# Kernel tuning notes

Measured on AMD Instinct MI355X. Metric: run time of the kernel, lower is better.

The kernel has to match this reference:

```python
import jax, jax.numpy as jnp
import numpy as np

B, D, OUT = 8192, 1024, 256
H1, H2 = 8, 4
EPS = 1e-5


def setup_inputs() -> dict:
    key = jax.random.key(0)
    ks = jax.random.split(key, 8)
    sc = lambda k, shape: jax.random.normal(k, shape, jnp.float32) * 0.05
    return {
        "x": jax.random.normal(ks[0], (B, D), jnp.float32),
        "W1": sc(ks[1], (D, H1, 1)),      # D diagonal blocks of the masked Linear(D -> 8D)
        "b1": sc(ks[2], (D * H1,)),
        "g1": jnp.ones((D * H1,), jnp.float32),
        "be1": jnp.zeros((D * H1,), jnp.float32),
        "W2": sc(ks[3], (D, H2, H1)),     # D diagonal blocks of the masked Linear(8D -> 4D)
        "b2": sc(ks[4], (D * H2,)),
        "g2": jnp.ones((D * H2,), jnp.float32),
        "be2": jnp.zeros((D * H2,), jnp.float32),
        "Wfc": sc(ks[5], (OUT, D * H2)),
        "bfc": sc(ks[6], (OUT,)),
    }


def _batchnorm(h, g, b):
    # BatchNorm1d in training mode: per-channel batch mean, biased variance
    mu = h.mean(axis=0)
    var = h.var(axis=0)  # ddof=0 (biased), matching torch normalization
    return g * (h - mu) * jax.lax.rsqrt(var + EPS) + b


def reference(x, W1, b1, g1, be1, W2, b2, g2, be2, Wfc, bfc):
    n = x.shape[0]
    # layer 1: per-feature (1 -> H1) block GEMM == masked dense Linear
    h = jnp.einsum("bdi,doi->bdo", x[:, :, None], W1).reshape(n, D * H1)
    h = jax.nn.relu(_batchnorm(h + b1, g1, be1))
    # layer 2: per-feature (H1 -> H2) block GEMM
    h = jnp.einsum("bdi,doi->bdo", h.reshape(n, D, H1), W2).reshape(n, D * H2)
    h = jax.nn.relu(_batchnorm(h + b2, g2, be2))
    # dense output head
    return h @ Wfc.T + bfc
```

## Files before the change

### kernel.cpp

```cpp
#include <hip/hip_runtime.h>

#define EPSV 1e-5f

typedef short bf16x8 __attribute__((ext_vector_type(8)));
typedef float f32x4 __attribute__((ext_vector_type(4)));

static __device__ __forceinline__ unsigned short f2b(float f) {
  union { float f; unsigned u; } v; v.f = f;
  return (unsigned short)((v.u + 0x7fffu + ((v.u >> 16) & 1u)) >> 16);
}

__global__ void k_pre(const float* __restrict__ wfc, unsigned short* __restrict__ wb,
                      const float* __restrict__ x, float* __restrict__ ps1) {
  if (blockIdx.x < 512) {
    const int f = blockIdx.x * 256 + threadIdx.x;
    const int l15 = f & 15, quad = (f >> 4) & 3, nb = (f >> 6) & 15, k32b = f >> 10;
    const int n = nb * 16 + l15;
    const int k = k32b * 32 + quad * 8;
    const float4* src = (const float4*)(wfc + (size_t)n * 4096 + k);
    float4 a = src[0], b = src[1];
    ushort4 o0, o1;
    o0.x = f2b(a.x); o0.y = f2b(a.y); o0.z = f2b(a.z); o0.w = f2b(a.w);
    o1.x = f2b(b.x); o1.y = f2b(b.y); o1.z = f2b(b.z); o1.w = f2b(b.w);
    *(ushort4*)(wb + (size_t)f * 8) = o0;
    *(ushort4*)(wb + (size_t)f * 8 + 4) = o1;
  } else {
    const int blk = blockIdx.x - 512;
    const int c = threadIdx.x * 4;
    const int r0 = blk * 32;
    float4 s = {0.f,0.f,0.f,0.f}, q = {0.f,0.f,0.f,0.f};
    for (int g = 0; g < 4; ++g) {
      float4 v[8];
#pragma unroll
      for (int j = 0; j < 8; ++j)
        v[j] = *(const float4*)(x + (size_t)(r0 + g*8 + j) * 1024 + c);
#pragma unroll
      for (int j = 0; j < 8; ++j) {
        s.x += v[j].x; s.y += v[j].y; s.z += v[j].z; s.w += v[j].w;
        q.x = fmaf(v[j].x, v[j].x, q.x); q.y = fmaf(v[j].y, v[j].y, q.y);
        q.z = fmaf(v[j].z, v[j].z, q.z); q.w = fmaf(v[j].w, v[j].w, q.w);
      }
    }
    *(float4*)(ps1 + (size_t)blk * 2048 + c) = s;
    *(float4*)(ps1 + (size_t)blk * 2048 + 1024 + c) = q;
  }
}

__global__ __launch_bounds__(256) void k_fin1(const float* __restrict__ ps1,
    const float* __restrict__ W1, const float* __restrict__ g1,
    const float* __restrict__ be1, float* __restrict__ pt) {
  __shared__ float redS[8][32], redQ[8][32];
  const int t = threadIdx.x;
  const int d0 = blockIdx.x * 32;
  const int dl = t & 31, slot = t >> 5;
  float s = 0.f, q = 0.f;
  for (int u = 0; u < 32; u += 8) {
#pragma unroll
    for (int w = 0; w < 8; ++w) {
      const size_t base = (size_t)(slot * 32 + u + w) * 2048 + d0 + dl;
      s += ps1[base];
      q += ps1[base + 1024];
    }
  }
  redS[slot][dl] = s; redQ[slot][dl] = q;
  __syncthreads();
  const int dloc = t >> 3, i = t & 7;
  float xs = 0.f, xq = 0.f;
#pragma unroll
  for (int p = 0; p < 8; ++p) { xs += redS[p][dloc]; xq += redQ[p][dloc]; }
  const float inv = 1.f / 8192.f;
  const int d = d0 + dloc;
  const int c = d * 8 + i;
  float mean = xs * inv;
  float var = xq * inv - mean * mean;
  float w = W1[c];
  float s1 = g1[c] * w * rsqrtf(w * w * var + EPSV);
  float t1 = be1[c] - s1 * mean;
  pt[(size_t)d * 56 + i] = s1;
  pt[(size_t)d * 56 + 8 + i] = t1;
}

__global__ __launch_bounds__(256) void k_stats2(const float* __restrict__ x,
    const float* __restrict__ pt, const float* __restrict__ W2,
    float* __restrict__ ps2s, float* __restrict__ ps2q) {
  __shared__ float red[8][32][8];
  const int t = threadIdx.x;
  const int dl = t & 31, slot = t >> 5;
  const int d = blockIdx.x * 32 + dl;
  float s1v[8], t1v[8], w2v[32];
  {
    const f32x4* pq = (const f32x4*)(pt + (size_t)d * 56);
    f32x4 a = pq[0], b = pq[1], c = pq[2], e = pq[3];
#pragma unroll
    for (int j = 0; j < 4; ++j) {
      s1v[j] = a[j]; s1v[4 + j] = b[j];
      t1v[j] = c[j]; t1v[4 + j] = e[j];
    }
  }
  const float4* wp = (const float4*)(W2 + (size_t)d * 32);
#pragma unroll
  for (int i = 0; i < 8; ++i) {
    float4 v = wp[i];
    w2v[i*4+0]=v.x; w2v[i*4+1]=v.y; w2v[i*4+2]=v.z; w2v[i*4+3]=v.w;
  }
  float s[4] = {0.f,0.f,0.f,0.f}, q[4] = {0.f,0.f,0.f,0.f};
  const int b0 = blockIdx.y * 256 + slot * 32;
  for (int r = 0; r < 32; r += 8) {
    float xv[8];
#pragma unroll
    for (int j = 0; j < 8; ++j)
      xv[j] = x[(size_t)(b0 + r + j) * 1024 + d];
#pragma unroll
    for (int j = 0; j < 8; ++j) {
      float a1[8];
#pragma unroll
      for (int i = 0; i < 8; ++i) a1[i] = fmaxf(fmaf(s1v[i], xv[j], t1v[i]), 0.f);
#pragma unroll
      for (int o = 0; o < 4; ++o) {
        float h = 0.f;
#pragma unroll
        for (int i = 0; i < 8; ++i) h = fmaf(a1[i], w2v[o*8+i], h);
        s[o] += h;
        q[o] = fmaf(h, h, q[o]);
      }
    }
  }
#pragma unroll
  for (int j = 0; j < 4; ++j) {
    red[slot][dl][j] = s[j];
    red[slot][dl][4+j] = q[j];
  }
  __syncthreads();
  const int d2l = t >> 3, j = t & 7;
  float v = 0.f;
#pragma unroll
  for (int p = 0; p < 8; ++p) v += red[p][d2l][j];
  const int c2 = (blockIdx.x * 32 + d2l) * 4 + (t & 3);
  if (j < 4) ps2s[(size_t)blockIdx.y * 4096 + c2] = v;
  else       ps2q[(size_t)blockIdx.y * 4096 + c2] = v;
}

__global__ void k_fin2(const float* __restrict__ W2, const float* __restrict__ g2,
                       const float* __restrict__ be2, const float* __restrict__ ps2s,
                       const float* __restrict__ ps2q, float* __restrict__ pt) {
  const int c2 = blockIdx.x * 256 + threadIdx.x;
  const int d = c2 >> 2, o = c2 & 3;
  float sm = 0.f, sq = 0.f;
#pragma unroll
  for (int b = 0; b < 32; ++b) {
    sm += ps2s[(size_t)b * 4096 + c2];
    sq += ps2q[(size_t)b * 4096 + c2];
  }
  const float inv = 1.f / 8192.f;
  float m = sm * inv;
  float var = sq * inv - m * m;
  float s2 = g2[c2] * rsqrtf(var + EPSV);
  float t2 = be2[c2] - s2 * m;
  pt[(size_t)d * 56 + 48 + o] = t2;
#pragma unroll
  for (int i = 0; i < 8; ++i)
    pt[(size_t)d * 56 + 16 + o * 8 + i] = W2[(size_t)d * 32 + o * 8 + i] * s2;
}

__global__ __launch_bounds__(256, 3) void k_gemm(const float* __restrict__ x,
    const float* __restrict__ pt, const unsigned short* __restrict__ wb,
    const float* __restrict__ bfc, float* __restrict__ out) {
  __shared__ __align__(16) unsigned short As[2][32 * 136];
  const int t = threadIdx.x;
  const int lane = t & 63;
  const int wv = t >> 6;
  const int m0 = blockIdx.x * 32;
  const int kQ = blockIdx.y;
  const int d0 = kQ * 256;
  const int quad = lane >> 4;
  const int l15 = lane & 15;
  const int dl = t & 31, bs = t >> 5;
  const int chrot = blockIdx.x & 7;

  f32x4 acc[2][4];
#pragma unroll
  for (int mt = 0; mt < 2; ++mt)
#pragma unroll
    for (int nt = 0; nt < 4; ++nt) {
      f32x4 z = {0.f, 0.f, 0.f, 0.f};
      acc[mt][nt] = z;
    }

  float pv[52];
  float xv[4];

#define PREFETCH(CH) do {                                                   \
    const int d_ = d0 + (CH) * 32 + dl;                                     \
    const f32x4* pp_ = (const f32x4*)(pt + (size_t)d_ * 56);                \
    _Pragma("unroll")                                                       \
    for (int i_ = 0; i_ < 13; ++i_) {                                       \
      f32x4 v_ = pp_[i_];                                                   \
      pv[i_*4+0] = v_[0]; pv[i_*4+1] = v_[1];                               \
      pv[i_*4+2] = v_[2]; pv[i_*4+3] = v_[3];                               \
    }                                                                       \
    _Pragma("unroll")                                                       \
    for (int r_ = 0; r_ < 4; ++r_)                                          \
      xv[r_] = x[(size_t)(m0 + bs * 4 + r_) * 1024 + d_];                   \
  } while (0)

#define GEN_TILE(NB) do {                                                   \
    _Pragma("unroll")                                                       \
    for (int r_ = 0; r_ < 4; ++r_) {                                        \
      const float xvv_ = xv[r_];                                            \
      float a1_[8];                                                         \
      _Pragma("unroll")                                                     \
      for (int i_ = 0; i_ < 8; ++i_)                                        \
        a1_[i_] = fmaxf(fmaf(pv[i_], xvv_, pv[8 + i_]), 0.f);               \
      unsigned short o4_[4];                                                \
      _Pragma("unroll")                                                     \
      for (int o_ = 0; o_ < 4; ++o_) {                                      \
        float h_ = pv[48 + o_];                                             \
        _Pragma("unroll")                                                   \
        for (int i_ = 0; i_ < 8; ++i_)                                      \
          h_ = fmaf(a1_[i_], pv[16 + o_ * 8 + i_], h_);                     \
        o4_[o_] = f2b(fmaxf(h_, 0.f));                                      \
      }                                                                     \
      *(ushort4*)&As[NB][(bs * 4 + r_) * 136 + dl * 4] =                    \
          make_ushort4(o4_[0], o4_[1], o4_[2], o4_[3]);                     \
    }                                                                       \
  } while (0)

  PREFETCH(chrot);
  GEN_TILE(0);
  __syncthreads();

  for (int chi = 0; chi < 8; ++chi) {
    const int cur = chi & 1;
    const int ch = (chi + chrot) & 7;
    if (chi + 1 < 8) {
      const int chn = (chi + 1 + chrot) & 7;
      PREFETCH(chn);
    }
#pragma unroll
    for (int kk = 0; kk < 4; ++kk) {
      bf16x8 af0 = *(const bf16x8*)&As[cur][l15 * 136 + kk * 32 + quad * 8];
      bf16x8 af1 = *(const bf16x8*)&As[cur][(16 + l15) * 136 + kk * 32 + quad * 8];
      const int k32b = kQ * 32 + ch * 4 + kk;
#pragma unroll
      for (int nt = 0; nt < 4; ++nt) {
        const int frag = k32b * 16 + wv * 4 + nt;
        bf16x8 bfr = *(const bf16x8*)&wb[((size_t)frag * 64 + lane) * 8];
        acc[0][nt] = __builtin_amdgcn_mfma_f32_16x16x32_bf16(af0, bfr, acc[0][nt], 0, 0, 0);
        acc[1][nt] = __builtin_amdgcn_mfma_f32_16x16x32_bf16(af1, bfr, acc[1][nt], 0, 0, 0);
      }
    }
    if (chi + 1 < 8) {
      GEN_TILE(cur ^ 1);
    }
    __syncthreads();
  }

#undef PREFETCH
#undef GEN_TILE

#pragma unroll
  for (int nt = 0; nt < 4; ++nt) {
    const int col = wv * 64 + nt * 16 + l15;
    const float bias = (kQ == 0) ? bfc[col] : 0.f;
#pragma unroll
    for (int mt = 0; mt < 2; ++mt) {
#pragma unroll
      for (int r = 0; r < 4; ++r) {
        const int row = m0 + mt * 16 + quad * 4 + r;
        atomicAdd(&out[(size_t)row * 256 + col], acc[mt][nt][r] + bias);
      }
    }
  }
}

extern "C" void kernel_launch(void* const* d_in, const int* in_sizes, int n_in,
                              void* d_out, int out_size, void* d_ws, size_t ws_size,
                              hipStream_t stream) {
  const float* x   = (const float*)d_in[0];
  const float* W1  = (const float*)d_in[1];
  const float* g1  = (const float*)d_in[3];
  const float* be1 = (const float*)d_in[4];
  const float* W2  = (const float*)d_in[5];
  const float* g2  = (const float*)d_in[7];
  const float* be2 = (const float*)d_in[8];
  const float* Wfc = (const float*)d_in[9];
  const float* bfc = (const float*)d_in[10];
  float* out = (float*)d_out;

  char* ws = (char*)d_ws;
  unsigned short* wb = (unsigned short*)ws;
  float* pt     = (float*)(ws + (2u << 20));
  float* shared = (float*)(ws + (2u << 20) + (256u << 10));
  float* ps1  = shared;
  float* ps2s = shared;
  float* ps2q = shared + 32 * 4096;

  hipMemsetAsync(d_out, 0, (size_t)out_size * sizeof(float), stream);

  k_pre   <<<dim3(768),    256, 0, stream>>>(Wfc, wb, x, ps1);
  k_fin1  <<<dim3(32),     256, 0, stream>>>(ps1, W1, g1, be1, pt);
  k_stats2<<<dim3(32, 32), 256, 0, stream>>>(x, pt, W2, ps2s, ps2q);
  k_fin2  <<<dim3(16),     256, 0, stream>>>(W2, g2, be2, ps2s, ps2q, pt);
  k_gemm  <<<dim3(256, 4), 256, 0, stream>>>(x, pt, wb, bfc, out);
}
```

Before: 188.5 us.

## Stage Wfc fragments in LDS via direct global-to-LDS loads and enlarge M tile

The GEMM kernel now covers 64 rows per block instead of 32 and walks 16 K-chunks of 64. Each chunk's bf16 Wfc fragments are loaded straight into a double-buffered LDS area with global_load_lds, so all four waves share them instead of each lane reading B from global memory. The larger M tile doubles reuse of each B fragment and halves the grid, which cuts total Wfc traffic. In exchange, the A tile is now single-buffered with two barriers per chunk, so generating A no longer overlaps the MFMAs. Occupancy is also lower: more LDS and 64 accumulator registers per thread, with launch bounds dropped to 2.

```diff
diff --git a/kernel.cpp b/kernel.cpp
--- a/kernel.cpp
+++ b/kernel.cpp
@@ -4,6 +4,8 @@
 
 typedef short bf16x8 __attribute__((ext_vector_type(8)));
 typedef float f32x4 __attribute__((ext_vector_type(4)));
+typedef const __attribute__((address_space(1))) unsigned int gu32;
+typedef __attribute__((address_space(3))) unsigned int lu32;
 
 static __device__ __forceinline__ unsigned short f2b(float f) {
   union { float f; unsigned u; } v; v.f = f;
@@ -162,108 +164,124 @@
     pt[(size_t)d * 56 + 16 + o * 8 + i] = W2[(size_t)d * 32 + o * 8 + i] * s2;
 }
 
-__global__ __launch_bounds__(256, 3) void k_gemm(const float* __restrict__ x,
+__global__ __launch_bounds__(256, 2) void k_gemm(const float* __restrict__ x,
     const float* __restrict__ pt, const unsigned short* __restrict__ wb,
     const float* __restrict__ bfc, float* __restrict__ out) {
-  __shared__ __align__(16) unsigned short As[2][32 * 136];
+  __shared__ __align__(16) unsigned short Bs[2][32 * 512];
+  __shared__ __align__(16) unsigned short As[64 * 72];
   const int t = threadIdx.x;
   const int lane = t & 63;
   const int wv = t >> 6;
-  const int m0 = blockIdx.x * 32;
+  const int m0 = blockIdx.x * 64;
   const int kQ = blockIdx.y;
-  const int d0 = kQ * 256;
   const int quad = lane >> 4;
   const int l15 = lane & 15;
-  const int dl = t & 31, bs = t >> 5;
-  const int chrot = blockIdx.x & 7;
-
-  f32x4 acc[2][4];
-#pragma unroll
-  for (int mt = 0; mt < 2; ++mt)
+  const int dloc = t & 15, rowg = t >> 4;
+  const int k32q = kQ * 32;
+
+  f32x4 acc[4][4];
+#pragma unroll
+  for (int mt = 0; mt < 4; ++mt)
 #pragma unroll
     for (int nt = 0; nt < 4; ++nt) {
       f32x4 z = {0.f, 0.f, 0.f, 0.f};
       acc[mt][nt] = z;
     }
 
-  float pv[52];
   float xv[4];
 
-#define PREFETCH(CH) do {                                                   \
-    const int d_ = d0 + (CH) * 32 + dl;                                     \
+#define STAGE_B(CH, BUF) do {                                               \
+    const int k32b0_ = k32q + (CH) * 2;                                     \
+    _Pragma("unroll")                                                       \
+    for (int j_ = 0; j_ < 8; ++j_) {                                        \
+      const int fl_ = j_ * 4 + wv;                                          \
+      const int gfrag_ = (k32b0_ + (fl_ >> 4)) * 16 + (fl_ & 15);           \
+      const unsigned short* gp_ = wb + ((size_t)gfrag_ * 64 + lane) * 8;    \
+      __builtin_amdgcn_global_load_lds((gu32*)gp_,                          \
+          (lu32*)&Bs[BUF][fl_ * 512], 16, 0, 0);                            \
+    }                                                                       \
+  } while (0)
+
+#define PRE_X(CH) do {                                                      \
+    const int d_ = kQ * 256 + (CH) * 16 + dloc;                             \
+    _Pragma("unroll")                                                       \
+    for (int r_ = 0; r_ < 4; ++r_)                                          \
+      xv[r_] = x[(size_t)(m0 + rowg * 4 + r_) * 1024 + d_];                 \
+  } while (0)
+
+#define GEN_A(CH) do {                                                      \
+    const int d_ = kQ * 256 + (CH) * 16 + dloc;                             \
     const f32x4* pp_ = (const f32x4*)(pt + (size_t)d_ * 56);                \
+    float pv_[52];                                                          \
     _Pragma("unroll")                                                       \
     for (int i_ = 0; i_ < 13; ++i_) {                                       \
       f32x4 v_ = pp_[i_];                                                   \
-      pv[i_*4+0] = v_[0]; pv[i_*4+1] = v_[1];                               \
-      pv[i_*4+2] = v_[2]; pv[i_*4+3] = v_[3];                               \
+      pv_[i_*4+0] = v_[0]; pv_[i_*4+1] = v_[1];                             \
+      pv_[i_*4+2] = v_[2]; pv_[i_*4+3] = v_[3];                             \
     }                                                                       \
-    _Pragma("unroll")                                                       \
-    for (int r_ = 0; r_ < 4; ++r_)                                          \
-      xv[r_] = x[(size_t)(m0 + bs * 4 + r_) * 1024 + d_];                   \
-  } while (0)
-
-#define GEN_TILE(NB) do {                                                   \
     _Pragma("unroll")                                                       \
     for (int r_ = 0; r_ < 4; ++r_) {                                        \
       const float xvv_ = xv[r_];                                            \
       float a1_[8];                                                         \
       _Pragma("unroll")                                                     \
       for (int i_ = 0; i_ < 8; ++i_)                                        \
-        a1_[i_] = fmaxf(fmaf(pv[i_], xvv_, pv[8 + i_]), 0.f);               \
+        a1_[i_] = fmaxf(fmaf(pv_[i_], xvv_, pv_[8 + i_]), 0.f);             \
       unsigned short o4_[4];                                                \
       _Pragma("unroll")                                                     \
       for (int o_ = 0; o_ < 4; ++o_) {                                      \
-        float h_ = pv[48 + o_];                                             \
+        float h_ = pv_[48 + o_];                                            \
         _Pragma("unroll")                                                   \
         for (int i_ = 0; i_ < 8; ++i_)                                      \
-          h_ = fmaf(a1_[i_], pv[16 + o_ * 8 + i_], h_);                     \
+          h_ = fmaf(a1_[i_], pv_[16 + o_ * 8 + i_], h_);                    \
         o4_[o_] = f2b(fmaxf(h_, 0.f));                                      \
       }                                                                     \
-      *(ushort4*)&As[NB][(bs * 4 + r_) * 136 + dl * 4] =                    \
+      *(ushort4*)&As[(rowg * 4 + r_) * 72 + dloc * 4] =                     \
           make_ushort4(o4_[0], o4_[1], o4_[2], o4_[3]);                     \
     }                                                                       \
   } while (0)
 
-  PREFETCH(chrot);
-  GEN_TILE(0);
+  STAGE_B(0, 0);
+  PRE_X(0);
+  GEN_A(0);
   __syncthreads();
 
-  for (int chi = 0; chi < 8; ++chi) {
+  for (int chi = 0; chi < 16; ++chi) {
     const int cur = chi & 1;
-    const int ch = (chi + chrot) & 7;
-    if (chi + 1 < 8) {
-      const int chn = (chi + 1 + chrot) & 7;
-      PREFETCH(chn);
-    }
-#pragma unroll
-    for (int kk = 0; kk < 4; ++kk) {
-      bf16x8 af0 = *(const bf16x8*)&As[cur][l15 * 136 + kk * 32 + quad * 8];
-      bf16x8 af1 = *(const bf16x8*)&As[cur][(16 + l15) * 136 + kk * 32 + quad * 8];
-      const int k32b = kQ * 32 + ch * 4 + kk;
+    if (chi < 15) PRE_X(chi + 1);
+#pragma unroll
+    for (int kk = 0; kk < 2; ++kk) {
+      bf16x8 af[4];
+#pragma unroll
+      for (int mt = 0; mt < 4; ++mt)
+        af[mt] = *(const bf16x8*)&As[(mt * 16 + l15) * 72 + kk * 32 + quad * 8];
 #pragma unroll
       for (int nt = 0; nt < 4; ++nt) {
-        const int frag = k32b * 16 + wv * 4 + nt;
-        bf16x8 bfr = *(const bf16x8*)&wb[((size_t)frag * 64 + lane) * 8];
-        acc[0][nt] = __builtin_amdgcn_mfma_f32_16x16x32_bf16(af0, bfr, acc[0][nt], 0, 0, 0);
-        acc[1][nt] = __builtin_amdgcn_mfma_f32_16x16x32_bf16(af1, bfr, acc[1][nt], 0, 0, 0);
+        const int fl = kk * 16 + wv * 4 + nt;
+        bf16x8 bfr = *(const bf16x8*)&Bs[cur][fl * 512 + lane * 8];
+#pragma unroll
+        for (int mt = 0; mt < 4; ++mt)
+          acc[mt][nt] = __builtin_amdgcn_mfma_f32_16x16x32_bf16(af[mt], bfr,
+                                                                acc[mt][nt], 0, 0, 0);
       }
     }
-    if (chi + 1 < 8) {
-      GEN_TILE(cur ^ 1);
-    }
     __syncthreads();
-  }
-
-#undef PREFETCH
-#undef GEN_TILE
+    if (chi < 15) {
+      STAGE_B(chi + 1, cur ^ 1);
+      GEN_A(chi + 1);
+    }
+    __syncthreads();
+  }
+
+#undef STAGE_B
+#undef PRE_X
+#undef GEN_A
 
 #pragma unroll
   for (int nt = 0; nt < 4; ++nt) {
     const int col = wv * 64 + nt * 16 + l15;
     const float bias = (kQ == 0) ? bfc[col] : 0.f;
 #pragma unroll
-    for (int mt = 0; mt < 2; ++mt) {
+    for (int mt = 0; mt < 4; ++mt) {
 #pragma unroll
       for (int r = 0; r < 4; ++r) {
         const int row = m0 + mt * 16 + quad * 4 + r;
@@ -301,5 +319,5 @@
   k_fin1  <<<dim3(32),     256, 0, stream>>>(ps1, W1, g1, be1, pt);
   k_stats2<<<dim3(32, 32), 256, 0, stream>>>(x, pt, W2, ps2s, ps2q);
   k_fin2  <<<dim3(16),     256, 0, stream>>>(W2, g2, be2, ps2s, ps2q, pt);
-  k_gemm  <<<dim3(256, 4), 256, 0, stream>>>(x, pt, wb, bfc, out);
-}
+  k_gemm  <<<dim3(128, 4), 256, 0, stream>>>(x, pt, wb, bfc, out);
+}
```

Result: faster. 181.7 us (-3.6%).
